# Performance work log

Measured on AMD Instinct MI355X. Metric: run time of the kernel, lower is better.

Reference implementation:

```python
import jax, jax.numpy as jnp
import numpy as np

L, C = 32768, 512
EPS = 1e-5

def _layernorm(x, w, b):
    mu = jnp.mean(x, axis=-1, keepdims=True)
    var = jnp.mean(jnp.square(x - mu), axis=-1, keepdims=True)
    return (x - mu) * jax.lax.rsqrt(var + EPS) * w + b

def _scan(u, decay):
    # inclusive first-order linear scan: b_t = decay * b_{t-1} + u_t
    a = jnp.broadcast_to(decay, u.shape)
    def combine(l, r):
        return (l[0] * r[0], r[1] + r[0] * l[1])
    _, b = jax.lax.associative_scan(combine, (a, u), axis=0)
    return b

def setup_inputs() -> dict:
    key = jax.random.key(0)
    ks = jax.random.split(key, 8)
    s = 0.02
    return {
        "x": jax.random.normal(ks[0], (L, C), dtype=jnp.float32),
        "ln1_w": jnp.ones((C,), jnp.float32),
        "ln1_b": jnp.zeros((C,), jnp.float32),
        "W_in": jax.random.normal(ks[1], (C, C), jnp.float32) * s,
        "b_in": jnp.zeros((C,), jnp.float32),
        "W_gate": jax.random.normal(ks[2], (C, C), jnp.float32) * s,
        "b_gate": jnp.zeros((C,), jnp.float32),
        "W_out": jax.random.normal(ks[3], (C, C), jnp.float32) * s,
        "b_out": jnp.zeros((C,), jnp.float32),
        "decay_logit": jnp.zeros((C,), jnp.float32),  # torch init: zeros -> sigmoid = 0.5
        "ln2_w": jnp.ones((C,), jnp.float32),
        "ln2_b": jnp.zeros((C,), jnp.float32),
        "W_ff1": jax.random.normal(ks[4], (C, 2 * C), jnp.float32) * s,
        "b_ff1": jnp.zeros((2 * C,), jnp.float32),
        "W_ff2": jax.random.normal(ks[5], (2 * C, C), jnp.float32) * s,
        "b_ff2": jnp.zeros((C,), jnp.float32),
    }

def reference(x, ln1_w, ln1_b, W_in, b_in, W_gate, b_gate, W_out, b_out,
              decay_logit, ln2_w, ln2_b, W_ff1, b_ff1, W_ff2, b_ff2):
    hidden = _layernorm(x, ln1_w, ln1_b)
    u = hidden @ W_in + b_in
    gate = jax.nn.sigmoid(hidden @ W_gate + b_gate)
    decay = jax.nn.sigmoid(decay_logit)
    fwd = _scan(u, decay) * gate
    bwd = jnp.flip(_scan(jnp.flip(u, axis=0), decay), axis=0) * gate
    state_out = 0.5 * (fwd + bwd)
    x = x + state_out @ W_out + b_out
    h = _layernorm(x, ln2_w, ln2_b)
    x = x + jax.nn.silu(h @ W_ff1 + b_ff1) @ W_ff2 + b_ff2
    return x
```

## Files before the change

kernel.cpp:

```cpp
#include <hip/hip_runtime.h>
#include <stdint.h>


#define L_SEQ 32768
#define CDIM 512
#define LN_EPS 1e-5f
#define CHUNK 64
#define NCHUNK (L_SEQ / CHUNK)

typedef __attribute__((ext_vector_type(8))) short short8;
typedef __attribute__((ext_vector_type(4))) float floatx4;

__device__ inline unsigned short f2bf(float f) {
  union { float f; unsigned int u; } v; v.f = f;
  unsigned int r = v.u + 0x7fffu + ((v.u >> 16) & 1u);
  return (unsigned short)(r >> 16);
}
__device__ inline float bf2f(unsigned short h) {
  union { float f; unsigned int u; } v; v.u = ((unsigned int)h) << 16;
  return v.f;
}
__device__ inline float sigmoidf_(float x) { return 1.0f / (1.0f + __expf(-x)); }

__global__ __launch_bounds__(256) void ln_kernel(const float* __restrict__ x,
    const float* __restrict__ w, const float* __restrict__ b,
    unsigned short* __restrict__ out) {
  int row = blockIdx.x * 4 + (threadIdx.x >> 6);
  int lane = threadIdx.x & 63;
  const float4* xr = (const float4*)(x + (size_t)row * CDIM);
  float4 v0 = xr[lane * 2];
  float4 v1 = xr[lane * 2 + 1];
  float s = v0.x + v0.y + v0.z + v0.w + v1.x + v1.y + v1.z + v1.w;
  float s2 = v0.x * v0.x + v0.y * v0.y + v0.z * v0.z + v0.w * v0.w +
             v1.x * v1.x + v1.y * v1.y + v1.z * v1.z + v1.w * v1.w;
  for (int m = 32; m > 0; m >>= 1) {
    s += __shfl_xor(s, m, 64);
    s2 += __shfl_xor(s2, m, 64);
  }
  float mean = s * (1.0f / CDIM);
  float var = s2 * (1.0f / CDIM) - mean * mean;
  float rs = rsqrtf(var + LN_EPS);
  const float4* wr = (const float4*)w;
  const float4* br = (const float4*)b;
  float4 w0 = wr[lane * 2], w1 = wr[lane * 2 + 1];
  float4 b0 = br[lane * 2], b1 = br[lane * 2 + 1];
  unsigned int p0 = (unsigned int)f2bf((v0.x - mean) * rs * w0.x + b0.x) |
                    ((unsigned int)f2bf((v0.y - mean) * rs * w0.y + b0.y) << 16);
  unsigned int p1 = (unsigned int)f2bf((v0.z - mean) * rs * w0.z + b0.z) |
                    ((unsigned int)f2bf((v0.w - mean) * rs * w0.w + b0.w) << 16);
  unsigned int p2 = (unsigned int)f2bf((v1.x - mean) * rs * w1.x + b1.x) |
                    ((unsigned int)f2bf((v1.y - mean) * rs * w1.y + b1.y) << 16);
  unsigned int p3 = (unsigned int)f2bf((v1.z - mean) * rs * w1.z + b1.z) |
                    ((unsigned int)f2bf((v1.w - mean) * rs * w1.w + b1.w) << 16);
  uint4 pk; pk.x = p0; pk.y = p1; pk.z = p2; pk.w = p3;
  *((uint4*)(out + (size_t)row * CDIM + lane * 8)) = pk;
}

__global__ __launch_bounds__(256) void prep_all(
    const float* __restrict__ W_in, const float* __restrict__ W_gate,
    const float* __restrict__ W_out, const float* __restrict__ W_ff1,
    const float* __restrict__ W_ff2, const float* __restrict__ logit,
    unsigned short* __restrict__ Wt_ig, unsigned short* __restrict__ Wt_out,
    unsigned short* __restrict__ Wt_ff1, unsigned short* __restrict__ Wt_ff2,
    float* __restrict__ decay, float* __restrict__ decayT) {
  int b = blockIdx.x;
  if (b >= 1792) {
    for (int c = threadIdx.x; c < CDIM; c += 256) {
      float d = sigmoidf_(logit[c]);
      decay[c] = d;
      float p = d;
      for (int i = 0; i < 6; i++) p *= p;
      decayT[c] = p;
    }
    return;
  }
  const float* W; unsigned short* Wt; int Kd, Nd, t;
  if (b < 256)       { W = W_in;   Wt = Wt_ig;             Kd = 512;  Nd = 512;  t = b; }
  else if (b < 512)  { W = W_gate; Wt = Wt_ig + 512 * 512; Kd = 512;  Nd = 512;  t = b - 256; }
  else if (b < 768)  { W = W_out;  Wt = Wt_out;            Kd = 512;  Nd = 512;  t = b - 512; }
  else if (b < 1280) { W = W_ff1;  Wt = Wt_ff1;            Kd = 512;  Nd = 1024; t = b - 768; }
  else               { W = W_ff2;  Wt = Wt_ff2;            Kd = 1024; Nd = 512;  t = b - 1280; }
  int ntx = Nd >> 5;
  int n0 = (t % ntx) * 32, k0 = (t / ntx) * 32;
  __shared__ float tile[32][33];
  int tx = threadIdx.x & 31, ty = threadIdx.x >> 5;
  for (int r = 0; r < 32; r += 8)
    tile[ty + r][tx] = W[(size_t)(k0 + ty + r) * Nd + n0 + tx];
  __syncthreads();
  for (int r = 0; r < 32; r += 8)
    Wt[(size_t)(n0 + ty + r) * Kd + k0 + tx] = f2bf(tile[tx][ty + r]);
}

template <int EPI>
__global__ __launch_bounds__(256, 3) void gemm_bt(
    const unsigned short* __restrict__ A, const unsigned short* __restrict__ Bt,
    const float* __restrict__ biasA, const float* __restrict__ biasB,
    const float* __restrict__ res, float* __restrict__ outF,
    unsigned short* __restrict__ outU, unsigned short* __restrict__ outG,
    int M, int N, int K) {
  __shared__ char smemRaw[34048];
  unsigned short* As = (unsigned short*)smemRaw;
  unsigned short* Bs = (unsigned short*)(smemRaw + 16384);

  int nbx = gridDim.x, nby = gridDim.y;
  int bid = blockIdx.x + blockIdx.y * nbx;
  int per = (nbx * nby) >> 3;
  int w = (bid & 7) * per + (bid >> 3);
  int ni = w % nby;
  int mi = w / nby;
  int bm = mi << 7, bn = ni << 7;

  int tid = threadIdx.x, wave = tid >> 6, lane = tid & 63;
  int wm = (wave >> 1) * 64, wn = (wave & 1) * 64;

  int srow = wave * 16 + (lane >> 2);
  int chunkSel = (lane & 3) ^ ((lane >> 3) & 3);
  int scol = chunkSel * 8;
  const unsigned short* aP0 = A + (size_t)(bm + srow) * K + scol;
  const unsigned short* aP1 = A + (size_t)(bm + 64 + srow) * K + scol;
  const unsigned short* bP0 = Bt + (size_t)(bn + srow) * K + scol;
  const unsigned short* bP1 = Bt + (size_t)(bn + 64 + srow) * K + scol;
  int wslot = wave * 512 + lane * 8;

  floatx4 acc[4][4];
#pragma unroll
  for (int i = 0; i < 4; i++)
#pragma unroll
    for (int j = 0; j < 4; j++) acc[i][j] = (floatx4){0.f, 0.f, 0.f, 0.f};

  int quad = lane >> 4, r16 = lane & 15;
  int cSwz = ((quad ^ (r16 >> 1)) & 3) * 8;

  int NK = K >> 5;
  uint4 pa0, pa1, pb0, pb1;
  uint4 qa0, qa1, qb0, qb1;

  pa0 = *(const uint4*)(aP0);
  pa1 = *(const uint4*)(aP1);
  pb0 = *(const uint4*)(bP0);
  pb1 = *(const uint4*)(bP1);
  *(uint4*)&As[wslot]        = pa0;
  *(uint4*)&As[2048 + wslot] = pa1;
  *(uint4*)&Bs[wslot]        = pb0;
  *(uint4*)&Bs[2048 + wslot] = pb1;
  pa0 = *(const uint4*)(aP0 + 32);
  pa1 = *(const uint4*)(aP1 + 32);
  pb0 = *(const uint4*)(bP0 + 32);
  pb1 = *(const uint4*)(bP1 + 32);
  __syncthreads();

  for (int k = 0; k < NK; ++k) {
    int cur = (k & 1) * 4096, nxt = cur ^ 4096;
    short8 af[4], bfm[4];
#pragma unroll
    for (int i = 0; i < 4; i++)
      af[i] = *(const short8*)(&As[cur + (wm + i * 16 + r16) * 32 + cSwz]);
#pragma unroll
    for (int j = 0; j < 4; j++)
      bfm[j] = *(const short8*)(&Bs[cur + (wn + j * 16 + r16) * 32 + cSwz]);
    if (k + 2 < NK) {
      int o = (k + 2) * 32;
      qa0 = *(const uint4*)(aP0 + o);
      qa1 = *(const uint4*)(aP1 + o);
      qb0 = *(const uint4*)(bP0 + o);
      qb1 = *(const uint4*)(bP1 + o);
    }
#pragma unroll
    for (int i = 0; i < 4; i++)
#pragma unroll
      for (int j = 0; j < 4; j++)
        acc[i][j] = __builtin_amdgcn_mfma_f32_16x16x32_bf16(af[i], bfm[j], acc[i][j], 0, 0, 0);
    if (k + 1 < NK) {
      *(uint4*)&As[nxt + wslot]        = pa0;
      *(uint4*)&As[nxt + 2048 + wslot] = pa1;
      *(uint4*)&Bs[nxt + wslot]        = pb0;
      *(uint4*)&Bs[nxt + 2048 + wslot] = pb1;
    }
    __syncthreads();
    pa0 = qa0; pa1 = qa1; pb0 = qb0; pb1 = qb1;
  }

  if (EPI == 1) {
#pragma unroll
    for (int j = 0; j < 4; j++) {
      int n = bn + wn + j * 16 + r16;
#pragma unroll
      for (int i = 0; i < 4; i++) {
        int mb = bm + wm + i * 16 + quad * 4;
#pragma unroll
        for (int r = 0; r < 4; r++) {
          size_t idx = (size_t)(mb + r) * N + n;
          outF[idx] = res[idx] + acc[i][j][r] + biasA[n];
        }
      }
    }
  } else {
    unsigned short* sm = (unsigned short*)smemRaw;
#pragma unroll
    for (int j = 0; j < 4; j++) {
      int n = bn + wn + j * 16 + r16;
      int ln = wn + j * 16 + r16;
#pragma unroll
      for (int i = 0; i < 4; i++) {
        int lmb = wm + i * 16 + quad * 4;
#pragma unroll
        for (int r = 0; r < 4; r++) {
          float v = acc[i][j][r];
          float t;
          if (EPI == 0) {
            t = (n < 512) ? (v + biasA[n]) : sigmoidf_(v + biasB[n - 512]);
          } else {
            float z = v + biasA[n];
            t = z * sigmoidf_(z);
          }
          sm[(lmb + r) * 132 + ln] = f2bf(t);
        }
      }
    }
    __syncthreads();
    int row = tid >> 1, half = tid & 1;
    const unsigned short* src = sm + row * 132 + half * 64;
    unsigned short* gptr;
    if (EPI == 0) {
      gptr = ((bn < 512) ? outU : (outG - 512)) + (size_t)(bm + row) * 512 + bn + half * 64;
    } else {
      gptr = outG + (size_t)(bm + row) * N + bn + half * 64;
    }
#pragma unroll
    for (int s = 0; s < 8; s++)
      *(short8*)(gptr + s * 8) = *(const short8*)(src + s * 8);
  }
}

__global__ __launch_bounds__(512) void scan_phase1(const unsigned short* __restrict__ u,
    const float* __restrict__ decay, float* __restrict__ fa, float* __restrict__ ba) {
  int c = threadIdx.x, k = blockIdx.x;
  float d = decay[c];
  const unsigned short* up = u + (size_t)k * CHUNK * CDIM + c;
  float f = 0.f, bs = 0.f, p = 1.f;
#pragma unroll 8
  for (int t = 0; t < CHUNK; t++) {
    float v = bf2f(up[(size_t)t * CDIM]);
    f = d * f + v;
    bs += p * v;
    p *= d;
  }
  fa[(size_t)k * CDIM + c] = f;
  ba[(size_t)k * CDIM + c] = bs;
}

__global__ __launch_bounds__(256) void scan_phase2(const float* __restrict__ fa,
    const float* __restrict__ ba, const float* __restrict__ decayT,
    float* __restrict__ fc, float* __restrict__ bc) {
  int c = blockIdx.x * 256 + threadIdx.x;
  float dT = decayT[c];
  float run = 0.f;
#pragma unroll 8
  for (int k = 0; k < NCHUNK; k++) {
    fc[(size_t)k * CDIM + c] = run;
    run = dT * run + fa[(size_t)k * CDIM + c];
  }
  run = 0.f;
#pragma unroll 8
  for (int k = NCHUNK - 1; k >= 0; k--) {
    bc[(size_t)k * CDIM + c] = run;
    run = dT * run + ba[(size_t)k * CDIM + c];
  }
}

__global__ __launch_bounds__(512) void scan_phase3(const unsigned short* __restrict__ u,
    const unsigned short* __restrict__ gate, const float* __restrict__ decay,
    const float* __restrict__ fc, const float* __restrict__ bc,
    unsigned short* __restrict__ state) {
  int c = threadIdx.x, k = blockIdx.x;
  float d = decay[c];
  size_t base = (size_t)k * CHUNK * CDIM + c;
  float fwd[CHUNK];
  float run = fc[(size_t)k * CDIM + c];
#pragma unroll
  for (int t = 0; t < CHUNK; t++) {
    run = d * run + bf2f(u[base + (size_t)t * CDIM]);
    fwd[t] = run;
  }
  float runb = bc[(size_t)k * CDIM + c];
#pragma unroll
  for (int t = CHUNK - 1; t >= 0; t--) {
    runb = d * runb + bf2f(u[base + (size_t)t * CDIM]);
    float g = bf2f(gate[base + (size_t)t * CDIM]);
    state[base + (size_t)t * CDIM] = f2bf(0.5f * (fwd[t] + runb) * g);
  }
}

extern "C" void kernel_launch(void* const* d_in, const int* in_sizes, int n_in,
                              void* d_out, int out_size, void* d_ws, size_t ws_size,
                              hipStream_t stream) {
  const float* x = (const float*)d_in[0];
  const float* ln1_w = (const float*)d_in[1];
  const float* ln1_b = (const float*)d_in[2];
  const float* W_in = (const float*)d_in[3];
  const float* b_in = (const float*)d_in[4];
  const float* W_gate = (const float*)d_in[5];
  const float* b_gate = (const float*)d_in[6];
  const float* W_out = (const float*)d_in[7];
  const float* b_out = (const float*)d_in[8];
  const float* decay_logit = (const float*)d_in[9];
  const float* ln2_w = (const float*)d_in[10];
  const float* ln2_b = (const float*)d_in[11];
  const float* W_ff1 = (const float*)d_in[12];
  const float* b_ff1 = (const float*)d_in[13];
  const float* W_ff2 = (const float*)d_in[14];
  const float* b_ff2 = (const float*)d_in[15];

  char* ws = (char*)d_ws;
  size_t off = 0;
  auto alloc = [&](size_t bytes) -> void* {
    void* p = ws + off;
    off += (bytes + 255) & ~(size_t)255;
    return p;
  };
  unsigned short* Wt_ig  = (unsigned short*)alloc((size_t)1024 * 512 * 2);
  unsigned short* Wt_out = (unsigned short*)alloc((size_t)512 * 512 * 2);
  unsigned short* Wt_ff1 = (unsigned short*)alloc((size_t)1024 * 512 * 2);
  unsigned short* Wt_ff2 = (unsigned short*)alloc((size_t)512 * 1024 * 2);
  float* fa = (float*)alloc((size_t)NCHUNK * CDIM * 4);
  float* ba = (float*)alloc((size_t)NCHUNK * CDIM * 4);
  float* fc = (float*)alloc((size_t)NCHUNK * CDIM * 4);
  float* bc = (float*)alloc((size_t)NCHUNK * CDIM * 4);
  float* decay  = (float*)alloc(CDIM * 4);
  float* decayT = (float*)alloc(CDIM * 4);
  const size_t LC2 = (size_t)L_SEQ * CDIM * 2;
  unsigned short* R1 = (unsigned short*)alloc(LC2);
  unsigned short* R2 = (unsigned short*)alloc(LC2);
  unsigned short* R3 = (unsigned short*)alloc(LC2);
  unsigned short* hidden = R1;
  unsigned short* state  = R1;
  unsigned short* hbuf   = R1;
  unsigned short* u_buf  = R2;
  unsigned short* gate   = R3;
  unsigned short* ffb    = R2;
  float* x2 = (float*)d_out;

  prep_all<<<1793, 256, 0, stream>>>(W_in, W_gate, W_out, W_ff1, W_ff2,
      decay_logit, Wt_ig, Wt_out, Wt_ff1, Wt_ff2, decay, decayT);

  ln_kernel<<<L_SEQ / 4, 256, 0, stream>>>(x, ln1_w, ln1_b, hidden);

  gemm_bt<0><<<dim3(L_SEQ / 128, 1024 / 128), 256, 0, stream>>>(
      hidden, Wt_ig, b_in, b_gate, nullptr, nullptr, u_buf, gate, L_SEQ, 1024, 512);

  scan_phase1<<<NCHUNK, 512, 0, stream>>>(u_buf, decay, fa, ba);
  scan_phase2<<<2, 256, 0, stream>>>(fa, ba, decayT, fc, bc);
  scan_phase3<<<NCHUNK, 512, 0, stream>>>(u_buf, gate, decay, fc, bc, state);

  gemm_bt<1><<<dim3(L_SEQ / 128, 512 / 128), 256, 0, stream>>>(
      state, Wt_out, b_out, nullptr, x, x2, nullptr, nullptr, L_SEQ, 512, 512);

  ln_kernel<<<L_SEQ / 4, 256, 0, stream>>>(x2, ln2_w, ln2_b, hbuf);

  gemm_bt<2><<<dim3(L_SEQ / 128, 1024 / 128), 256, 0, stream>>>(
      hbuf, Wt_ff1, b_ff1, nullptr, nullptr, nullptr, nullptr, ffb, L_SEQ, 1024, 512);

  gemm_bt<1><<<dim3(L_SEQ / 128, 512 / 128), 256, 0, stream>>>(
      ffb, Wt_ff2, b_ff2, nullptr, x2, x2, nullptr, nullptr, L_SEQ, 512, 1024);
}
```

Before: 489.6 us.

## Rewrite GEMM as 256x256 tile with direct global-to-LDS four-stage pipeline

Replaces the 128x128, 256-thread GEMM with a 256x256 tile, 512-thread kernel. Operand tiles are copied straight from global memory into LDS with global_load_lds through a 4-slot ring buffer, gated by explicit vmcnt waits, and MFMA sections are wrapped in setprio. This is meant to raise data reuse per tile and hide load latency without staging through registers, at the cost of 128KB of LDS, fewer blocks per CU and a two-pass epilogue. The scan phase2 forward and backward loops are also fused into one loop for more memory-level parallelism.

```diff
diff --git a/kernel.cpp b/kernel.cpp
--- a/kernel.cpp
+++ b/kernel.cpp
@@ -21,6 +21,12 @@
   return v.f;
 }
 __device__ inline float sigmoidf_(float x) { return 1.0f / (1.0f + __expf(-x)); }
+
+__device__ __forceinline__ void gll16(const void* g, void* l) {
+  __builtin_amdgcn_global_load_lds(
+      (__attribute__((address_space(1))) void*)g,
+      (__attribute__((address_space(3))) void*)l, 16, 0, 0);
+}
 
 __global__ __launch_bounds__(256) void ln_kernel(const float* __restrict__ x,
     const float* __restrict__ w, const float* __restrict__ b,
@@ -92,143 +98,147 @@
 }
 
 template <int EPI>
-__global__ __launch_bounds__(256, 3) void gemm_bt(
+__global__ __launch_bounds__(512, 2) void gemm256(
     const unsigned short* __restrict__ A, const unsigned short* __restrict__ Bt,
     const float* __restrict__ biasA, const float* __restrict__ biasB,
     const float* __restrict__ res, float* __restrict__ outF,
     unsigned short* __restrict__ outU, unsigned short* __restrict__ outG,
     int M, int N, int K) {
-  __shared__ char smemRaw[34048];
-  unsigned short* As = (unsigned short*)smemRaw;
-  unsigned short* Bs = (unsigned short*)(smemRaw + 16384);
+  __shared__ unsigned short smem[65536];
+  unsigned short* As = smem;
+  unsigned short* Bs = smem + 32768;
 
   int nbx = gridDim.x, nby = gridDim.y;
   int bid = blockIdx.x + blockIdx.y * nbx;
   int per = (nbx * nby) >> 3;
   int w = (bid & 7) * per + (bid >> 3);
-  int ni = w % nby;
-  int mi = w / nby;
-  int bm = mi << 7, bn = ni << 7;
+  int ni = w % nby, mi = w / nby;
+  int bm = mi << 8, bn = ni << 8;
 
   int tid = threadIdx.x, wave = tid >> 6, lane = tid & 63;
-  int wm = (wave >> 1) * 64, wn = (wave & 1) * 64;
-
-  int srow = wave * 16 + (lane >> 2);
-  int chunkSel = (lane & 3) ^ ((lane >> 3) & 3);
-  int scol = chunkSel * 8;
-  const unsigned short* aP0 = A + (size_t)(bm + srow) * K + scol;
-  const unsigned short* aP1 = A + (size_t)(bm + 64 + srow) * K + scol;
-  const unsigned short* bP0 = Bt + (size_t)(bn + srow) * K + scol;
-  const unsigned short* bP1 = Bt + (size_t)(bn + 64 + srow) * K + scol;
-  int wslot = wave * 512 + lane * 8;
-
-  floatx4 acc[4][4];
-#pragma unroll
-  for (int i = 0; i < 4; i++)
+  int wm = (wave >> 2) * 128, wn = (wave & 3) * 64;
+  int quad = lane >> 4, r16 = lane & 15;
+
+  int sr = tid >> 2;
+  int sc = tid & 3;
+  int swz = (sr >> 1) & 3;
+  const unsigned short* aSrc0 = A + (size_t)(bm + sr) * K + ((sc ^ swz) * 8);
+  const unsigned short* aSrc1 = aSrc0 + (size_t)128 * K;
+  const unsigned short* bSrc0 = Bt + (size_t)(bn + sr) * K + ((sc ^ swz) * 8);
+  const unsigned short* bSrc1 = bSrc0 + (size_t)128 * K;
+  int ldsW = wave * 512;
+
+#define STAGE(slot, ktile) do {                                   \
+    int _o = (ktile) * 32;                                        \
+    unsigned short* _a = As + (slot) * 8192 + ldsW;               \
+    unsigned short* _b = Bs + (slot) * 8192 + ldsW;               \
+    gll16(aSrc0 + _o, _a);                                        \
+    gll16(aSrc1 + _o, _a + 4096);                                 \
+    gll16(bSrc0 + _o, _b);                                        \
+    gll16(bSrc1 + _o, _b + 4096);                                 \
+  } while (0)
+
+  floatx4 acc[8][4];
+#pragma unroll
+  for (int i = 0; i < 8; i++)
 #pragma unroll
     for (int j = 0; j < 4; j++) acc[i][j] = (floatx4){0.f, 0.f, 0.f, 0.f};
 
-  int quad = lane >> 4, r16 = lane & 15;
-  int cSwz = ((quad ^ (r16 >> 1)) & 3) * 8;
+  int cOff = ((quad ^ ((r16 >> 1) & 3)) & 3) * 8;
+  int aBase = (wm + r16) * 32 + cOff;
+  int bBase = (wn + r16) * 32 + cOff;
 
   int NK = K >> 5;
-  uint4 pa0, pa1, pb0, pb1;
-  uint4 qa0, qa1, qb0, qb1;
-
-  pa0 = *(const uint4*)(aP0);
-  pa1 = *(const uint4*)(aP1);
-  pb0 = *(const uint4*)(bP0);
-  pb1 = *(const uint4*)(bP1);
-  *(uint4*)&As[wslot]        = pa0;
-  *(uint4*)&As[2048 + wslot] = pa1;
-  *(uint4*)&Bs[wslot]        = pb0;
-  *(uint4*)&Bs[2048 + wslot] = pb1;
-  pa0 = *(const uint4*)(aP0 + 32);
-  pa1 = *(const uint4*)(aP1 + 32);
-  pb0 = *(const uint4*)(bP0 + 32);
-  pb1 = *(const uint4*)(bP1 + 32);
-  __syncthreads();
-
-  for (int k = 0; k < NK; ++k) {
-    int cur = (k & 1) * 4096, nxt = cur ^ 4096;
-    short8 af[4], bfm[4];
-#pragma unroll
-    for (int i = 0; i < 4; i++)
-      af[i] = *(const short8*)(&As[cur + (wm + i * 16 + r16) * 32 + cSwz]);
-#pragma unroll
-    for (int j = 0; j < 4; j++)
-      bfm[j] = *(const short8*)(&Bs[cur + (wn + j * 16 + r16) * 32 + cSwz]);
-    if (k + 2 < NK) {
-      int o = (k + 2) * 32;
-      qa0 = *(const uint4*)(aP0 + o);
-      qa1 = *(const uint4*)(aP1 + o);
-      qb0 = *(const uint4*)(bP0 + o);
-      qb1 = *(const uint4*)(bP1 + o);
+
+  STAGE(0, 0); STAGE(1, 1); STAGE(2, 2);
+  asm volatile("s_waitcnt vmcnt(8)" ::: "memory");
+  __builtin_amdgcn_s_barrier();
+  asm volatile("" ::: "memory");
+
+  for (int j = 0; j < NK; ++j) {
+    int slot = j & 3;
+    if (j + 3 < NK) STAGE((j + 3) & 3, j + 3);
+    const unsigned short* as = As + slot * 8192;
+    const unsigned short* bs = Bs + slot * 8192;
+    short8 af[8], bfr[4];
+#pragma unroll
+    for (int i = 0; i < 8; i++) af[i] = *(const short8*)(as + aBase + i * 512);
+#pragma unroll
+    for (int jj = 0; jj < 4; jj++) bfr[jj] = *(const short8*)(bs + bBase + jj * 512);
+    if (j + 1 < NK) {
+      asm volatile("s_waitcnt lgkmcnt(0)" ::: "memory");
+      if (j + 3 < NK)      asm volatile("s_waitcnt vmcnt(8)" ::: "memory");
+      else if (j + 2 < NK) asm volatile("s_waitcnt vmcnt(4)" ::: "memory");
+      else                 asm volatile("s_waitcnt vmcnt(0)" ::: "memory");
+      __builtin_amdgcn_s_barrier();
+      asm volatile("" ::: "memory");
     }
-#pragma unroll
-    for (int i = 0; i < 4; i++)
-#pragma unroll
-      for (int j = 0; j < 4; j++)
-        acc[i][j] = __builtin_amdgcn_mfma_f32_16x16x32_bf16(af[i], bfm[j], acc[i][j], 0, 0, 0);
-    if (k + 1 < NK) {
-      *(uint4*)&As[nxt + wslot]        = pa0;
-      *(uint4*)&As[nxt + 2048 + wslot] = pa1;
-      *(uint4*)&Bs[nxt + wslot]        = pb0;
-      *(uint4*)&Bs[nxt + 2048 + wslot] = pb1;
-    }
-    __syncthreads();
-    pa0 = qa0; pa1 = qa1; pb0 = qb0; pb1 = qb1;
-  }
+    __builtin_amdgcn_s_setprio(1);
+#pragma unroll
+    for (int i = 0; i < 8; i++)
+#pragma unroll
+      for (int jj = 0; jj < 4; jj++)
+        acc[i][jj] = __builtin_amdgcn_mfma_f32_16x16x32_bf16(af[i], bfr[jj], acc[i][jj], 0, 0, 0);
+    __builtin_amdgcn_s_setprio(0);
+  }
+#undef STAGE
 
   if (EPI == 1) {
 #pragma unroll
-    for (int j = 0; j < 4; j++) {
-      int n = bn + wn + j * 16 + r16;
-#pragma unroll
-      for (int i = 0; i < 4; i++) {
-        int mb = bm + wm + i * 16 + quad * 4;
+    for (int i = 0; i < 8; i++) {
+      int mb = bm + wm + i * 16 + quad * 4;
+#pragma unroll
+      for (int jj = 0; jj < 4; jj++) {
+        int n = bn + wn + jj * 16 + r16;
+        float bA = biasA[n];
 #pragma unroll
         for (int r = 0; r < 4; r++) {
           size_t idx = (size_t)(mb + r) * N + n;
-          outF[idx] = res[idx] + acc[i][j][r] + biasA[n];
+          outF[idx] = res[idx] + acc[i][jj][r] + bA;
         }
       }
     }
   } else {
-    unsigned short* sm = (unsigned short*)smemRaw;
-#pragma unroll
-    for (int j = 0; j < 4; j++) {
-      int n = bn + wn + j * 16 + r16;
-      int ln = wn + j * 16 + r16;
-#pragma unroll
-      for (int i = 0; i < 4; i++) {
-        int lmb = wm + i * 16 + quad * 4;
-#pragma unroll
-        for (int r = 0; r < 4; r++) {
-          float v = acc[i][j][r];
-          float t;
-          if (EPI == 0) {
-            t = (n < 512) ? (v + biasA[n]) : sigmoidf_(v + biasB[n - 512]);
-          } else {
-            float z = v + biasA[n];
-            t = z * sigmoidf_(z);
+    unsigned short* sm16 = smem;
+    for (int p = 0; p < 2; ++p) {
+      __syncthreads();
+#pragma unroll
+      for (int jj = 0; jj < 4; jj++) {
+        int colL = wn + jj * 16 + r16;
+        int n = bn + colL;
+#pragma unroll
+        for (int i = 0; i < 4; i++) {
+          int ii = p * 4 + i;
+          int lr = (wm >> 1) + i * 16 + quad * 4;
+#pragma unroll
+          for (int r = 0; r < 4; r++) {
+            float v = acc[ii][jj][r];
+            float t;
+            if (EPI == 0) {
+              t = (n < 512) ? (v + biasA[n]) : sigmoidf_(v + biasB[n - 512]);
+            } else {
+              float z = v + biasA[n];
+              t = z * sigmoidf_(z);
+            }
+            sm16[(lr + r) * 260 + colL] = f2bf(t);
           }
-          sm[(lmb + r) * 132 + ln] = f2bf(t);
         }
       }
+      __syncthreads();
+      int row = tid >> 2, c0 = (tid & 3) * 64;
+      int gr = bm + (row & 63) + ((row >> 6) * 128) + p * 64;
+      const unsigned short* srcp = sm16 + row * 260 + c0;
+      unsigned short* gptr;
+      if (EPI == 0) {
+        gptr = (bn < 512) ? (outU + (size_t)gr * 512 + bn + c0)
+                          : (outG + (size_t)gr * 512 + (bn - 512) + c0);
+      } else {
+        gptr = outG + (size_t)gr * N + bn + c0;
+      }
+#pragma unroll
+      for (int s = 0; s < 8; s++)
+        *(short8*)(gptr + s * 8) = *(const short8*)(srcp + s * 8);
     }
-    __syncthreads();
-    int row = tid >> 1, half = tid & 1;
-    const unsigned short* src = sm + row * 132 + half * 64;
-    unsigned short* gptr;
-    if (EPI == 0) {
-      gptr = ((bn < 512) ? outU : (outG - 512)) + (size_t)(bm + row) * 512 + bn + half * 64;
-    } else {
-      gptr = outG + (size_t)(bm + row) * N + bn + half * 64;
-    }
-#pragma unroll
-    for (int s = 0; s < 8; s++)
-      *(short8*)(gptr + s * 8) = *(const short8*)(src + s * 8);
   }
 }
 
@@ -254,17 +264,14 @@
     float* __restrict__ fc, float* __restrict__ bc) {
   int c = blockIdx.x * 256 + threadIdx.x;
   float dT = decayT[c];
-  float run = 0.f;
-#pragma unroll 8
+  float runf = 0.f, runb = 0.f;
+#pragma unroll 4
   for (int k = 0; k < NCHUNK; k++) {
-    fc[(size_t)k * CDIM + c] = run;
-    run = dT * run + fa[(size_t)k * CDIM + c];
-  }
-  run = 0.f;
-#pragma unroll 8
-  for (int k = NCHUNK - 1; k >= 0; k--) {
-    bc[(size_t)k * CDIM + c] = run;
-    run = dT * run + ba[(size_t)k * CDIM + c];
+    int kb = NCHUNK - 1 - k;
+    fc[(size_t)k * CDIM + c] = runf;
+    runf = dT * runf + fa[(size_t)k * CDIM + c];
+    bc[(size_t)kb * CDIM + c] = runb;
+    runb = dT * runb + ba[(size_t)kb * CDIM + c];
   }
 }
 
@@ -345,21 +352,21 @@
 
   ln_kernel<<<L_SEQ / 4, 256, 0, stream>>>(x, ln1_w, ln1_b, hidden);
 
-  gemm_bt<0><<<dim3(L_SEQ / 128, 1024 / 128), 256, 0, stream>>>(
+  gemm256<0><<<dim3(L_SEQ / 256, 1024 / 256), 512, 0, stream>>>(
       hidden, Wt_ig, b_in, b_gate, nullptr, nullptr, u_buf, gate, L_SEQ, 1024, 512);
 
   scan_phase1<<<NCHUNK, 512, 0, stream>>>(u_buf, decay, fa, ba);
   scan_phase2<<<2, 256, 0, stream>>>(fa, ba, decayT, fc, bc);
   scan_phase3<<<NCHUNK, 512, 0, stream>>>(u_buf, gate, decay, fc, bc, state);
 
-  gemm_bt<1><<<dim3(L_SEQ / 128, 512 / 128), 256, 0, stream>>>(
+  gemm256<1><<<dim3(L_SEQ / 256, 512 / 256), 512, 0, stream>>>(
       state, Wt_out, b_out, nullptr, x, x2, nullptr, nullptr, L_SEQ, 512, 512);
 
   ln_kernel<<<L_SEQ / 4, 256, 0, stream>>>(x2, ln2_w, ln2_b, hbuf);
 
-  gemm_bt<2><<<dim3(L_SEQ / 128, 1024 / 128), 256, 0, stream>>>(
+  gemm256<2><<<dim3(L_SEQ / 256, 1024 / 256), 512, 0, stream>>>(
       hbuf, Wt_ff1, b_ff1, nullptr, nullptr, nullptr, nullptr, ffb, L_SEQ, 1024, 512);
 
-  gemm_bt<1><<<dim3(L_SEQ / 128, 512 / 128), 256, 0, stream>>>(
+  gemm256<1><<<dim3(L_SEQ / 256, 512 / 256), 512, 0, stream>>>(
       ffb, Wt_ff2, b_ff2, nullptr, x2, x2, nullptr, nullptr, L_SEQ, 512, 1024);
 }
```

After: 622.0 us. 27.0% more time.

## Stage GEMM tiles with direct global-to-LDS loads and interleave scan phase2

Applied to the files above, without the earlier changes.

The GEMM main loop now uses global_load_lds to copy A/B tiles straight into shared memory instead of going through registers. This removes the register staging buffers, so the launch-bounds occupancy hint is raised from 3 to 4 blocks. The prefetch distance shrinks from two tiles to one, and a full vmcnt wait is added before each barrier, which may expose more load latency. Scan phase2 also interleaves the forward and backward chunk recurrences in one loop to get more independent memory operations in flight.

```diff
diff --git a/kernel.cpp b/kernel.cpp
--- a/kernel.cpp
+++ b/kernel.cpp
@@ -21,6 +21,12 @@
   return v.f;
 }
 __device__ inline float sigmoidf_(float x) { return 1.0f / (1.0f + __expf(-x)); }
+
+__device__ __forceinline__ void gll16(const void* g, void* l) {
+  __builtin_amdgcn_global_load_lds(
+      (__attribute__((address_space(1))) void*)g,
+      (__attribute__((address_space(3))) void*)l, 16, 0, 0);
+}
 
 __global__ __launch_bounds__(256) void ln_kernel(const float* __restrict__ x,
     const float* __restrict__ w, const float* __restrict__ b,
@@ -92,7 +98,7 @@
 }
 
 template <int EPI>
-__global__ __launch_bounds__(256, 3) void gemm_bt(
+__global__ __launch_bounds__(256, 4) void gemm_bt(
     const unsigned short* __restrict__ A, const unsigned short* __restrict__ Bt,
     const float* __restrict__ biasA, const float* __restrict__ biasB,
     const float* __restrict__ res, float* __restrict__ outF,
@@ -120,7 +126,15 @@
   const unsigned short* aP1 = A + (size_t)(bm + 64 + srow) * K + scol;
   const unsigned short* bP0 = Bt + (size_t)(bn + srow) * K + scol;
   const unsigned short* bP1 = Bt + (size_t)(bn + 64 + srow) * K + scol;
-  int wslot = wave * 512 + lane * 8;
+  int wbase = wave * 512;
+
+#define STAGE(bufOff, ktile) do {                                 \
+    int _o = (ktile) * 32;                                        \
+    gll16(aP0 + _o, As + (bufOff) + wbase);                       \
+    gll16(aP1 + _o, As + (bufOff) + 2048 + wbase);                \
+    gll16(bP0 + _o, Bs + (bufOff) + wbase);                       \
+    gll16(bP1 + _o, Bs + (bufOff) + 2048 + wbase);                \
+  } while (0)
 
   floatx4 acc[4][4];
 #pragma unroll
@@ -132,25 +146,14 @@
   int cSwz = ((quad ^ (r16 >> 1)) & 3) * 8;
 
   int NK = K >> 5;
-  uint4 pa0, pa1, pb0, pb1;
-  uint4 qa0, qa1, qb0, qb1;
-
-  pa0 = *(const uint4*)(aP0);
-  pa1 = *(const uint4*)(aP1);
-  pb0 = *(const uint4*)(bP0);
-  pb1 = *(const uint4*)(bP1);
-  *(uint4*)&As[wslot]        = pa0;
-  *(uint4*)&As[2048 + wslot] = pa1;
-  *(uint4*)&Bs[wslot]        = pb0;
-  *(uint4*)&Bs[2048 + wslot] = pb1;
-  pa0 = *(const uint4*)(aP0 + 32);
-  pa1 = *(const uint4*)(aP1 + 32);
-  pb0 = *(const uint4*)(bP0 + 32);
-  pb1 = *(const uint4*)(bP1 + 32);
+
+  STAGE(0, 0);
+  asm volatile("s_waitcnt vmcnt(0)" ::: "memory");
   __syncthreads();
 
   for (int k = 0; k < NK; ++k) {
     int cur = (k & 1) * 4096, nxt = cur ^ 4096;
+    if (k + 1 < NK) STAGE(nxt, k + 1);
     short8 af[4], bfm[4];
 #pragma unroll
     for (int i = 0; i < 4; i++)
@@ -158,27 +161,15 @@
 #pragma unroll
     for (int j = 0; j < 4; j++)
       bfm[j] = *(const short8*)(&Bs[cur + (wn + j * 16 + r16) * 32 + cSwz]);
-    if (k + 2 < NK) {
-      int o = (k + 2) * 32;
-      qa0 = *(const uint4*)(aP0 + o);
-      qa1 = *(const uint4*)(aP1 + o);
-      qb0 = *(const uint4*)(bP0 + o);
-      qb1 = *(const uint4*)(bP1 + o);
-    }
 #pragma unroll
     for (int i = 0; i < 4; i++)
 #pragma unroll
       for (int j = 0; j < 4; j++)
         acc[i][j] = __builtin_amdgcn_mfma_f32_16x16x32_bf16(af[i], bfm[j], acc[i][j], 0, 0, 0);
-    if (k + 1 < NK) {
-      *(uint4*)&As[nxt + wslot]        = pa0;
-      *(uint4*)&As[nxt + 2048 + wslot] = pa1;
-      *(uint4*)&Bs[nxt + wslot]        = pb0;
-      *(uint4*)&Bs[nxt + 2048 + wslot] = pb1;
-    }
+    asm volatile("s_waitcnt vmcnt(0)" ::: "memory");
     __syncthreads();
-    pa0 = qa0; pa1 = qa1; pb0 = qb0; pb1 = qb1;
-  }
+  }
+#undef STAGE
 
   if (EPI == 1) {
 #pragma unroll
@@ -254,17 +245,14 @@
     float* __restrict__ fc, float* __restrict__ bc) {
   int c = blockIdx.x * 256 + threadIdx.x;
   float dT = decayT[c];
-  float run = 0.f;
-#pragma unroll 8
+  float runf = 0.f, runb = 0.f;
+#pragma unroll 4
   for (int k = 0; k < NCHUNK; k++) {
-    fc[(size_t)k * CDIM + c] = run;
-    run = dT * run + fa[(size_t)k * CDIM + c];
-  }
-  run = 0.f;
-#pragma unroll 8
-  for (int k = NCHUNK - 1; k >= 0; k--) {
-    bc[(size_t)k * CDIM + c] = run;
-    run = dT * run + ba[(size_t)k * CDIM + c];
+    int kb = NCHUNK - 1 - k;
+    fc[(size_t)k * CDIM + c] = runf;
+    runf = dT * runf + fa[(size_t)k * CDIM + c];
+    bc[(size_t)kb * CDIM + c] = runb;
+    runb = dT * runb + ba[(size_t)kb * CDIM + c];
   }
 }
 
```

New measurement: 466.6 us. 1.05x faster.
